# Optimization experiments

Hardware: AMD Instinct MI355X
Metric: run time of the kernel (lower is better)

## Reference

```python
import jax, jax.numpy as jnp
import numpy as np

K = 49        # k_neighbors
EPS = 1e-5    # BatchNorm2d eps


def setup_inputs() -> dict:
    key = jax.random.key(0)
    ks = jax.random.split(key, 2)
    B, C, M, O = 64, 64, 32, 128
    X = jax.random.normal(ks[0], (B, C, M, M), dtype=jnp.float32)
    # conv1x1 weight (kaiming fan_out) flattened to (O, C); bias init 0
    W = jax.random.normal(ks[1], (O, C), dtype=jnp.float32) * (2.0 / O) ** 0.5
    b = jnp.zeros((O,), jnp.float32)
    gamma = jnp.ones((O,), jnp.float32)
    beta = jnp.zeros((O,), jnp.float32)
    run_mean = jnp.zeros((O,), jnp.float32)
    run_var = jnp.ones((O,), jnp.float32)
    return dict(X=X, W=W, b=b, gamma=gamma, beta=beta,
                run_mean=run_mean, run_var=run_var)


def _knn_aggregate(x):
    """x: (N, C) node features -> D^{-1/2} A D^{-1/2} x for the kNN graph."""
    N = x.shape[0]
    sq = jnp.sum(x * x, axis=1)
    d2 = sq[:, None] + sq[None, :] - 2.0 * (x @ x.T)
    dist = jnp.sqrt(jnp.maximum(d2, 0.0))              # torch.cdist (p=2)
    i = jnp.arange(N)
    dist = dist.at[i, i].set(jnp.inf)                  # fill_diagonal_(inf)
    _, knn = jax.lax.top_k(-dist, K)                   # (N, K) nearest indices
    # topk indices are distinct -> every row degree == K, and the column
    # normalizer uses the col node's row degree (also K), so
    # D^{-1/2} A D^{-1/2} x == mean of gathered neighbors.
    nb = x[knn]                                        # (N, K, C) gather
    return nb.sum(axis=1) / K


def reference(X, W, b, gamma, beta, run_mean, run_var):
    B, C, M, _ = X.shape
    N = M * M
    x = X.reshape(B, C, N).transpose(0, 2, 1)          # (B, N, C) nodes
    Z = jax.vmap(_knn_aggregate)(x)                    # (B, N, C) sparse GCN agg
    # 1x1 conv over the (M, M) grid == per-node linear map
    Fg = jnp.einsum('oc,bnc->bon', W, Z) + b[None, :, None]   # (B, O, N)
    Fg = jax.nn.relu(Fg)
    # BatchNorm2d with running stats (eval mode); Dropout2d is identity in eval
    inv = jax.lax.rsqrt(run_var + EPS)
    Fg = gamma[None, :, None] * (Fg - run_mean[None, :, None]) * inv[None, :, None] + beta[None, :, None]
    return Fg.mean(axis=2)                             # AdaptiveAvgPool2d(1) -> (B, O)
```

## Files before the change

kernel.cpp:

```cpp
#include <hip/hip_runtime.h>
#include <stdint.h>

#define BATCH 64
#define CDIM  64
#define NPTS  1024
#define ODIM  128
#define KNN   49
#define KNNP  52
#define BNEPS 1e-5f

typedef __attribute__((ext_vector_type(8))) short bf16x8;
typedef __attribute__((ext_vector_type(4))) float f32x4;

#define O_XF   0
#define SZ_XF  (BATCH*64*2*64*8*4)
#define O_SQ   (O_XF + SZ_XF)
#define SZ_SQ  (BATCH*NPTS*4)
#define O_KNN  (O_SQ + SZ_SQ)
#define SZ_KNN (BATCH*NPTS*KNNP*4)
#define O_Z    (O_KNN + SZ_KNN)
#define SZ_Z   (BATCH*NPTS*CDIM*4)
#define WS_NEED ((size_t)(O_Z + SZ_Z))

__global__ void gcn_init(const float* __restrict__ gamma, const float* __restrict__ beta,
                         const float* __restrict__ rmean, const float* __restrict__ rvar,
                         float* __restrict__ out) {
    int i = blockIdx.x * 256 + threadIdx.x;
    if (i < BATCH * ODIM) {
        int o = i & (ODIM - 1);
        out[i] = beta[o] - gamma[o] * rmean[o] * rsqrtf(rvar[o] + BNEPS);
    }
}

__global__ __launch_bounds__(256) void k0_split(const float* __restrict__ X,
                                                uint32_t* __restrict__ XF,
                                                float* __restrict__ sq) {
    const int b    = blockIdx.x >> 4;
    const int t16  = (blockIdx.x & 15) * 4 + (threadIdx.x >> 6);
    const int lane = threadIdx.x & 63;
    const int n    = t16 * 16 + (lane & 15);
    const int cg   = lane >> 4;
    const float* Xb = X + (size_t)b * CDIM * NPTS;
    float s = 0.f;
    for (int ks = 0; ks < 2; ks++) {
        uint32_t hi[4], lo[4];
#pragma unroll
        for (int dj = 0; dj < 4; dj++) {
            uint32_t hw[2], lw[2];
#pragma unroll
            for (int e = 0; e < 2; e++) {
                int c = ks * 32 + cg * 8 + dj * 2 + e;
                float x = Xb[(size_t)c * NPTS + n];
                s += x * x;
                uint32_t u  = __float_as_uint(x);
                uint32_t hr = (u + 0x7FFFu + ((u >> 16) & 1u)) >> 16;
                float    hf = __uint_as_float(hr << 16);
                uint32_t ul = __float_as_uint(x - hf);
                uint32_t lr = (ul + 0x7FFFu + ((ul >> 16) & 1u)) >> 16;
                hw[e] = hr; lw[e] = lr;
            }
            hi[dj] = hw[0] | (hw[1] << 16);
            lo[dj] = lw[0] | (lw[1] << 16);
        }
        size_t entry = ((size_t)(b * 64 + t16) * 2 + ks) * 64 + lane;
        uint32_t* p = XF + entry * 8;
        *(uint4*)p       = make_uint4(hi[0], hi[1], hi[2], hi[3]);
        *(uint4*)(p + 4) = make_uint4(lo[0], lo[1], lo[2], lo[3]);
    }
    s += __shfl_xor(s, 16, 64);
    s += __shfl_xor(s, 32, 64);
    if (lane < 16) sq[b * NPTS + n] = s;
}

__global__ __launch_bounds__(256, 4) void k1_gram_select(const uint32_t* __restrict__ XF,
                                                         const float* __restrict__ sq,
                                                         int* __restrict__ knn) {
    __shared__ uint32_t s_pk[8 * 1024];
    const int b    = blockIdx.x >> 6;
    const int rt   = blockIdx.x & 63;
    const int wave = threadIdx.x >> 6, lane = threadIdx.x & 63;
    const int q = lane >> 4, l15 = lane & 15;

    bf16x8 ahi[2], alo[2];
#pragma unroll
    for (int ks = 0; ks < 2; ks++) {
        const uint32_t* p = XF + (((size_t)(b * 64 + rt) * 2 + ks) * 64 + lane) * 8;
        ahi[ks] = *(const bf16x8*)p;
        alo[ks] = *(const bf16x8*)(p + 4);
    }
    const float* sqb = sq + b * NPTS;
    const int swq = (q & 1) << 4;

#pragma unroll
    for (int tt = 0; tt < 16; tt++) {
        const int t16 = wave * 16 + tt;
        f32x4 acc = {0.f, 0.f, 0.f, 0.f};
#pragma unroll
        for (int ks = 0; ks < 2; ks++) {
            const uint32_t* p = XF + (((size_t)(b * 64 + t16) * 2 + ks) * 64 + lane) * 8;
            bf16x8 bhi = *(const bf16x8*)p;
            bf16x8 blo = *(const bf16x8*)(p + 4);
            acc = __builtin_amdgcn_mfma_f32_16x16x32_bf16(ahi[ks], bhi, acc, 0, 0, 0);
            acc = __builtin_amdgcn_mfma_f32_16x16x32_bf16(alo[ks], bhi, acc, 0, 0, 0);
            acc = __builtin_amdgcn_mfma_f32_16x16x32_bf16(ahi[ks], blo, acc, 0, 0, 0);
        }
        const int col  = t16 * 16 + l15;
        const float sqv = sqb[col];
        float d[4];
#pragma unroll
        for (int i = 0; i < 4; i++)
            d[i] = fmaf(-2.f, acc[i], sqv);
        if (t16 == rt) {
#pragma unroll
            for (int i = 0; i < 4; i++)
                if (l15 == q * 4 + i) d[i] = __uint_as_float(0x7F800000u);
        }
        uint32_t key[4];
#pragma unroll
        for (int i = 0; i < 4; i++) {
            uint32_t u = __float_as_uint(d[i]);
            key[i] = u ^ (uint32_t)(((int)u >> 31) | 0x80000000);
        }
        uint32_t pk01 = __builtin_amdgcn_perm(key[1], key[0], 0x07060302);
        uint32_t pk23 = __builtin_amdgcn_perm(key[3], key[2], 0x07060302);
        s_pk[(2 * q) * 1024 + (col ^ swq)]     = pk01;
        s_pk[(2 * q + 1) * 1024 + (col ^ swq)] = pk23;
    }
    __syncthreads();

    uint32_t k[4][16];
    {
        const int swr = (wave & 1) << 4;
#pragma unroll
        for (int tt = 0; tt < 16; tt++) {
            uint32_t a  = s_pk[(2 * wave) * 1024 + ((tt * 64 + lane) ^ swr)];
            uint32_t bb = s_pk[(2 * wave + 1) * 1024 + ((tt * 64 + lane) ^ swr)];
            k[0][tt] = a & 0xFFFFu;  k[1][tt] = a >> 16;
            k[2][tt] = bb & 0xFFFFu; k[3][tt] = bb >> 16;
        }
    }

    uint32_t lo[4], hi[4];
    {
        uint32_t lmin[4];
#pragma unroll
        for (int r = 0; r < 4; r++) {
            uint32_t m = k[r][0];
#pragma unroll
            for (int tt = 1; tt < 16; tt++) m = k[r][tt] < m ? k[r][tt] : m;
            lmin[r] = m;
        }
#pragma unroll
        for (int r = 0; r < 4; r++) { lo[r] = lmin[r]; hi[r] = lmin[r]; }
#pragma unroll
        for (int off = 1; off < 64; off <<= 1) {
#pragma unroll
            for (int r = 0; r < 4; r++) {
                uint32_t a = (uint32_t)__shfl_xor((int)lo[r], off, 64);
                uint32_t m = (uint32_t)__shfl_xor((int)hi[r], off, 64);
                lo[r] = a < lo[r] ? a : lo[r];
                hi[r] = m > hi[r] ? m : hi[r];
            }
        }
    }

    for (int it = 0; it < 16; it++) {
        bool act0 = lo[0] < hi[0], act1 = lo[1] < hi[1];
        bool act2 = lo[2] < hi[2], act3 = lo[3] < hi[3];
        if (!act0 && !act1 && !act2 && !act3) break;
        uint32_t mid[4];
        int cnt[4] = {0, 0, 0, 0};
#pragma unroll
        for (int r = 0; r < 4; r++) mid[r] = (lo[r] + hi[r]) >> 1;
#pragma unroll
        for (int tt = 0; tt < 16; tt++) {
            cnt[0] += __popcll(__ballot(k[0][tt] <= mid[0]));
            cnt[1] += __popcll(__ballot(k[1][tt] <= mid[1]));
            cnt[2] += __popcll(__ballot(k[2][tt] <= mid[2]));
            cnt[3] += __popcll(__ballot(k[3][tt] <= mid[3]));
        }
#pragma unroll
        for (int r = 0; r < 4; r++)
            if (lo[r] < hi[r]) {
                if (cnt[r] >= KNN) hi[r] = mid[r]; else lo[r] = mid[r] + 1;
            }
    }

#pragma unroll
    for (int r = 0; r < 4; r++) {
        const uint32_t vstar = lo[r];
        int loc_lt = 0, loc_eq = 0;
#pragma unroll
        for (int tt = 0; tt < 16; tt++) {
            loc_lt += (k[r][tt] < vstar);
            loc_eq += (k[r][tt] == vstar);
        }
        uint32_t v = (uint32_t)loc_lt | ((uint32_t)loc_eq << 16);
#pragma unroll
        for (int off = 1; off < 64; off <<= 1) {
            uint32_t u = (uint32_t)__shfl_up((int)v, off, 64);
            if (lane >= off) v += u;
        }
        uint32_t tot = (uint32_t)__shfl((int)v, 63, 64);
        const int total_lt = (int)(tot & 0xFFFFu);
        int p_lt = (int)(v & 0xFFFFu) - loc_lt;
        int p_eq = total_lt + ((int)(v >> 16) - loc_eq);
        int* kout = knn + ((size_t)b * NPTS + rt * 16 + 4 * wave + r) * KNNP;
#pragma unroll
        for (int tt = 0; tt < 16; tt++) {
            bool islt = k[r][tt] < vstar;
            bool iseq = k[r][tt] == vstar;
            int pos = islt ? p_lt : p_eq;
            bool wv = islt || (iseq && p_eq < KNN);
            if (wv) kout[pos] = tt * 64 + lane;
            p_lt += islt; p_eq += iseq;
        }
    }
}

__global__ __launch_bounds__(512) void k2a_aggregate(const float* __restrict__ X,
                                                     const int* __restrict__ knn,
                                                     float* __restrict__ z) {
    __shared__ float XT[16 * 1024];
    const int b = blockIdx.x >> 2, cg = blockIdx.x & 3;
    const int t = threadIdx.x;
    const float* Xb = X + ((size_t)b * CDIM + cg * 16) * NPTS;
#pragma unroll
    for (int nn = 0; nn < 2; nn++) {
        int n = nn * 512 + t;
#pragma unroll
        for (int g = 0; g < 4; g++) {
            float4 v;
            v.x = Xb[(size_t)(4 * g + 0) * NPTS + n];
            v.y = Xb[(size_t)(4 * g + 1) * NPTS + n];
            v.z = Xb[(size_t)(4 * g + 2) * NPTS + n];
            v.w = Xb[(size_t)(4 * g + 3) * NPTS + n];
            int qp = g ^ ((n >> 1) & 3);
            *(float4*)&XT[n * 16 + qp * 4] = v;
        }
    }
    __syncthreads();
    const int wave = t >> 6, lane = t & 63;
    const int r2 = lane >> 4, kb = (lane >> 2) & 3, g = lane & 3;
    for (int rr = 0; rr < 32; rr++) {
        const int row = wave * 128 + rr * 4 + r2;
        const int* kr = knn + ((size_t)b * NPTS + row) * KNNP;
        float4 s = {0.f, 0.f, 0.f, 0.f};
#pragma unroll
        for (int cs = 0; cs < 3; cs++) {
            int4 j4 = *(const int4*)&kr[(kb + 4 * cs) * 4];
            int js[4] = {j4.x, j4.y, j4.z, j4.w};
#pragma unroll
            for (int e = 0; e < 4; e++) {
                int j = js[e];
                float4 v = *(const float4*)&XT[j * 16 + ((g ^ ((j >> 1) & 3)) << 2)];
                s.x += v.x; s.y += v.y; s.z += v.z; s.w += v.w;
            }
        }
        if (kb == 0) {
            int j = kr[48];
            float4 v = *(const float4*)&XT[j * 16 + ((g ^ ((j >> 1) & 3)) << 2)];
            s.x += v.x; s.y += v.y; s.z += v.z; s.w += v.w;
        }
#pragma unroll
        for (int off = 4; off <= 8; off <<= 1) {
            s.x += __shfl_xor(s.x, off, 64);
            s.y += __shfl_xor(s.y, off, 64);
            s.z += __shfl_xor(s.z, off, 64);
            s.w += __shfl_xor(s.w, off, 64);
        }
        if (kb == 0)
            *(float4*)&z[((size_t)b * NPTS + row) * CDIM + cg * 16 + g * 4] = s;
    }
}

__global__ __launch_bounds__(256) void k2b_gemm(const float* __restrict__ z,
                                                const float* __restrict__ W,
                                                const float* __restrict__ bias,
                                                const float* __restrict__ gamma,
                                                const float* __restrict__ rvar,
                                                float* __restrict__ out) {
    __shared__ __align__(16) float s_zz[128 * 64];
    __shared__ float s_red[2][256];
    const int b = blockIdx.x >> 3, nq = blockIdx.x & 7;
    const int t = threadIdx.x;
    const float* zb = z + ((size_t)b * NPTS + nq * 128) * CDIM;
#pragma unroll
    for (int qq = 0; qq < 8; qq++) {
        int e = qq * 256 + t;
        *(float4*)&s_zz[e * 4] = *(const float4*)&zb[e * 4];
    }
    __syncthreads();
    const int o2 = t & 63, h = t >> 6;
    float4 w0[16], w1[16];
#pragma unroll
    for (int c4 = 0; c4 < 16; c4++) {
        w0[c4] = *(const float4*)&W[(size_t)o2 * CDIM + c4 * 4];
        w1[c4] = *(const float4*)&W[(size_t)(o2 + 64) * CDIM + c4 * 4];
    }
    const float b0 = bias[o2], b1 = bias[o2 + 64];
    float r0 = 0.f, r1 = 0.f;
    for (int r = 0; r < 32; r++) {
        const float* zr = &s_zz[(h * 32 + r) * 64];
        float a0 = 0.f, a1 = 0.f;
#pragma unroll
        for (int c4 = 0; c4 < 16; c4++) {
            float4 zv = *(const float4*)&zr[c4 * 4];
            a0 += w0[c4].x * zv.x + w0[c4].y * zv.y + w0[c4].z * zv.z + w0[c4].w * zv.w;
            a1 += w1[c4].x * zv.x + w1[c4].y * zv.y + w1[c4].z * zv.z + w1[c4].w * zv.w;
        }
        r0 += fmaxf(a0 * (1.f / KNN) + b0, 0.f);
        r1 += fmaxf(a1 * (1.f / KNN) + b1, 0.f);
    }
    s_red[0][t] = r0; s_red[1][t] = r1;
    __syncthreads();
    if (t < 128) {
        const int oo = t & 63, which = t >> 6;
        const int o = which * 64 + oo;
        float sum = s_red[which][oo] + s_red[which][64 + oo] +
                    s_red[which][128 + oo] + s_red[which][192 + oo];
        float scale = gamma[o] * rsqrtf(rvar[o] + BNEPS) * (1.f / NPTS);
        atomicAdd(&out[b * ODIM + o], sum * scale);
    }
}

#define RTILE 8
#define APAD  1028
#define WPAD  132
#define POOLF (64 * WPAD)

__global__ __launch_bounds__(256) void gcn_main(
    const float* __restrict__ X, const float* __restrict__ W,
    const float* __restrict__ bias, const float* __restrict__ gamma,
    const float* __restrict__ rvar, float* __restrict__ out)
{
    __shared__ __align__(16) float s_pool[POOLF];
    __shared__ __align__(16) float s_fstage[4][APAD];
    __shared__ int   s_knn[RTILE][KNN];
    __shared__ float s_z[RTILE][CDIM];

    const int t = threadIdx.x;
    const int b = blockIdx.x >> 7;
    const int rtile = blockIdx.x & 127;
    const int r0 = rtile * RTILE;
    const float* Xb = X + (size_t)b * CDIM * NPTS;

    float acc[RTILE][4];
    float sqv[4];
#pragma unroll
    for (int r = 0; r < RTILE; r++)
#pragma unroll
        for (int u = 0; u < 4; u++) acc[r][u] = 0.f;
#pragma unroll
    for (int u = 0; u < 4; u++) sqv[u] = 0.f;

    for (int ch = 0; ch < 16; ch++) {
        const int c0 = ch * 4;
#pragma unroll
        for (int cc = 0; cc < 4; cc++) {
            float4 v = *(const float4*)(Xb + (size_t)(c0 + cc) * NPTS + 4 * t);
            *(float4*)&s_fstage[cc][4 * t] = v;
        }
        __syncthreads();
#pragma unroll
        for (int cc = 0; cc < 4; cc++) {
            float4 bv4 = *(const float4*)&s_fstage[cc][4 * t];
            float bv[4] = {bv4.x, bv4.y, bv4.z, bv4.w};
#pragma unroll
            for (int u = 0; u < 4; u++) sqv[u] += bv[u] * bv[u];
            const float* arow = Xb + (size_t)(c0 + cc) * NPTS + r0;
            float4 a0 = *(const float4*)(arow);
            float4 a1 = *(const float4*)(arow + 4);
            float av[8] = {a0.x, a0.y, a0.z, a0.w, a1.x, a1.y, a1.z, a1.w};
#pragma unroll
            for (int r = 0; r < RTILE; r++)
#pragma unroll
                for (int u = 0; u < 4; u++) acc[r][u] += av[r] * bv[u];
        }
        __syncthreads();
    }

    float* s_dist = s_pool;
#pragma unroll
    for (int r = 0; r < RTILE; r++) {
        const int rG = r0 + r;
        float d[4];
#pragma unroll
        for (int u = 0; u < 4; u++) {
            float dd = sqv[u] - 2.f * acc[r][u];
            d[u] = (4 * t + u == rG) ? __uint_as_float(0x7F800000u) : dd;
        }
        *(float4*)&s_dist[r * NPTS + 4 * t] = make_float4(d[0], d[1], d[2], d[3]);
    }
    __syncthreads();

    const int wave = t >> 6, lane = t & 63;
    const unsigned long long ltmask = (1ull << lane) - 1ull;
    for (int rr = 0; rr < 2; rr++) {
        const int row = wave * 2 + rr;
        unsigned key[16];
#pragma unroll
        for (int tt = 0; tt < 16; tt++) {
            unsigned u = __float_as_uint(s_dist[row * NPTS + tt * 64 + lane]);
            key[tt] = (u & 0x80000000u) ? ~u : (u | 0x80000000u);
        }
        unsigned lo = 0u, hi = 0xFFFFFFFFu;
        while (lo < hi) {
            unsigned mid = lo + ((hi - lo) >> 1);
            int cnt = 0;
#pragma unroll
            for (int tt = 0; tt < 16; tt++)
                cnt += __popcll(__ballot(key[tt] <= mid));
            if (cnt >= KNN) hi = mid; else lo = mid + 1;
        }
        const unsigned v49 = lo;
        int cntless = 0;
#pragma unroll
        for (int tt = 0; tt < 16; tt++)
            cntless += __popcll(__ballot(key[tt] < v49));
        const int need = KNN - cntless;
        int base = 0, eqtaken = 0;
#pragma unroll
        for (int tt = 0; tt < 16; tt++) {
            bool islt = key[tt] < v49;
            bool iseq = key[tt] == v49;
            unsigned long long meq = __ballot(iseq);
            int eqrank = eqtaken + __popcll(meq & ltmask);
            bool sel = islt || (iseq && (eqrank < need));
            unsigned long long msel = __ballot(sel);
            if (sel) {
                int pos = base + __popcll(msel & ltmask);
                s_knn[row][pos] = tt * 64 + lane;
            }
            base    += __popcll(msel);
            eqtaken += __popcll(meq);
        }
    }
    __syncthreads();

    float* astage = s_pool;
    float* s_redf = (float*)s_fstage;
    const int ar = t >> 5, acc8 = (t & 31) >> 2, ks = t & 3;
    for (int c0 = 0; c0 < CDIM; c0 += 8) {
#pragma unroll
        for (int qq = 0; qq < 8; qq++) {
            int if4 = qq * 256 + t;
            int cc = if4 >> 8, j4 = if4 & 255;
            float4 v = *(const float4*)(Xb + (size_t)(c0 + cc) * NPTS + 4 * j4);
            *(float4*)&astage[cc * APAD + 4 * j4] = v;
        }
        __syncthreads();
        float partial = 0.f;
        for (int k = ks; k < KNN; k += 4)
            partial += astage[acc8 * APAD + s_knn[ar][k]];
        s_redf[t] = partial;
        __syncthreads();
        if (t < 64) {
            int r = t >> 3, cc = t & 7;
            int bi = r * 32 + cc * 4;
            s_z[r][c0 + cc] = s_redf[bi] + s_redf[bi + 1] + s_redf[bi + 2] + s_redf[bi + 3];
        }
        __syncthreads();
    }

    float* wt = s_pool;
#pragma unroll 4
    for (int qq = 0; qq < 32; qq++) {
        int e = qq * 256 + t;
        int o = e >> 6, c = e & 63;
        wt[c * WPAD + o] = W[e];
    }
    __syncthreads();
    const int o = t & 127, rg = t >> 7;
    float facc[4] = {0.f, 0.f, 0.f, 0.f};
    for (int c = 0; c < CDIM; c += 4) {
        float w0 = wt[(c + 0) * WPAD + o], w1 = wt[(c + 1) * WPAD + o];
        float w2 = wt[(c + 2) * WPAD + o], w3 = wt[(c + 3) * WPAD + o];
#pragma unroll
        for (int qq = 0; qq < 4; qq++) {
            float4 zv = *(const float4*)&s_z[rg * 4 + qq][c];
            facc[qq] += w0 * zv.x + w1 * zv.y + w2 * zv.z + w3 * zv.w;
        }
    }
    const float bo = bias[o];
    float rsum = 0.f;
#pragma unroll
    for (int qq = 0; qq < 4; qq++) {
        float f = facc[qq] * (1.f / KNN) + bo;
        rsum += fmaxf(f, 0.f);
    }
    s_redf[t] = rsum;
    __syncthreads();
    if (t < 128) {
        float scale = gamma[t] * rsqrtf(rvar[t] + BNEPS) * (1.f / NPTS);
        atomicAdd(&out[b * ODIM + t], (s_redf[t] + s_redf[t + 128]) * scale);
    }
}

extern "C" void kernel_launch(void* const* d_in, const int* in_sizes, int n_in,
                              void* d_out, int out_size, void* d_ws, size_t ws_size,
                              hipStream_t stream) {
    const float* X     = (const float*)d_in[0];
    const float* W     = (const float*)d_in[1];
    const float* bias  = (const float*)d_in[2];
    const float* gamma = (const float*)d_in[3];
    const float* beta  = (const float*)d_in[4];
    const float* rmean = (const float*)d_in[5];
    const float* rvar  = (const float*)d_in[6];
    float* out = (float*)d_out;

    gcn_init<<<(BATCH * ODIM + 255) / 256, 256, 0, stream>>>(gamma, beta, rmean, rvar, out);
    if (ws_size >= WS_NEED) {
        uint8_t* ws = (uint8_t*)d_ws;
        uint32_t* XF  = (uint32_t*)(ws + O_XF);
        float*    sqw = (float*)(ws + O_SQ);
        int*      knn = (int*)(ws + O_KNN);
        float*    zw  = (float*)(ws + O_Z);
        k0_split<<<BATCH * 16, 256, 0, stream>>>(X, XF, sqw);
        k1_gram_select<<<BATCH * 64, 256, 0, stream>>>(XF, sqw, knn);
        k2a_aggregate<<<BATCH * 4, 512, 0, stream>>>(X, knn, zw);
        k2b_gemm<<<BATCH * 8, 256, 0, stream>>>(zw, W, bias, gamma, rvar, out);
    } else {
        gcn_main<<<BATCH * (NPTS / RTILE), 256, 0, stream>>>(X, W, bias, gamma, rvar, out);
    }
}
```

Measured before the change: 285.7 us.

## Fuse aggregate+GEMM, merge init into split, widen gram-select blocks with ballot-based emit

Folds the output-initialisation kernel into k0_split and fuses the neighbour aggregation with the 1x1-conv GEMM, so the Z intermediate no longer round-trips through global memory. k1_gram_select now handles two 16-row tiles per 512-thread block, which reuses the loaded B fragments across both tiles. Its index emission changes from a shuffle prefix scan to ballot/mbcnt positions, staged in LDS and written out with coalesced int4 stores. The trade-off is that the fused kernel reloads X once per 8-channel slice and does more serial work per block.

```diff
diff --git a/kernel.cpp b/kernel.cpp
--- a/kernel.cpp
+++ b/kernel.cpp
@@ -12,15 +12,18 @@
 typedef __attribute__((ext_vector_type(8))) short bf16x8;
 typedef __attribute__((ext_vector_type(4))) float f32x4;
 
+__device__ __forceinline__ int mbcnt64(unsigned long long m) {
+    return __builtin_amdgcn_mbcnt_hi((uint32_t)(m >> 32),
+           __builtin_amdgcn_mbcnt_lo((uint32_t)m, 0));
+}
+
 #define O_XF   0
 #define SZ_XF  (BATCH*64*2*64*8*4)
 #define O_SQ   (O_XF + SZ_XF)
 #define SZ_SQ  (BATCH*NPTS*4)
 #define O_KNN  (O_SQ + SZ_SQ)
 #define SZ_KNN (BATCH*NPTS*KNNP*4)
-#define O_Z    (O_KNN + SZ_KNN)
-#define SZ_Z   (BATCH*NPTS*CDIM*4)
-#define WS_NEED ((size_t)(O_Z + SZ_Z))
+#define WS_NEED ((size_t)(O_KNN + SZ_KNN))
 
 __global__ void gcn_init(const float* __restrict__ gamma, const float* __restrict__ beta,
                          const float* __restrict__ rmean, const float* __restrict__ rvar,
@@ -34,7 +37,17 @@
 
 __global__ __launch_bounds__(256) void k0_split(const float* __restrict__ X,
                                                 uint32_t* __restrict__ XF,
-                                                float* __restrict__ sq) {
+                                                float* __restrict__ sq,
+                                                const float* __restrict__ gamma,
+                                                const float* __restrict__ beta,
+                                                const float* __restrict__ rmean,
+                                                const float* __restrict__ rvar,
+                                                float* __restrict__ out) {
+    if (blockIdx.x < 32) {
+        int i = blockIdx.x * 256 + threadIdx.x;
+        int o = i & (ODIM - 1);
+        out[i] = beta[o] - gamma[o] * rmean[o] * rsqrtf(rvar[o] + BNEPS);
+    }
     const int b    = blockIdx.x >> 4;
     const int t16  = (blockIdx.x & 15) * 4 + (threadIdx.x >> 6);
     const int lane = threadIdx.x & 63;
@@ -72,86 +85,92 @@
     if (lane < 16) sq[b * NPTS + n] = s;
 }
 
-__global__ __launch_bounds__(256, 4) void k1_gram_select(const uint32_t* __restrict__ XF,
-                                                         const float* __restrict__ sq,
-                                                         int* __restrict__ knn) {
-    __shared__ uint32_t s_pk[8 * 1024];
-    const int b    = blockIdx.x >> 6;
-    const int rt   = blockIdx.x & 63;
+__global__ __launch_bounds__(512) void k1_gram_select(const uint32_t* __restrict__ XF,
+                                                      const float* __restrict__ sq,
+                                                      int* __restrict__ knn) {
+    __shared__ uint32_t s_pk[16 * 1024];
+    const int b    = blockIdx.x >> 5;
+    const int rt   = blockIdx.x & 31;
     const int wave = threadIdx.x >> 6, lane = threadIdx.x & 63;
     const int q = lane >> 4, l15 = lane & 15;
 
-    bf16x8 ahi[2], alo[2];
-#pragma unroll
-    for (int ks = 0; ks < 2; ks++) {
-        const uint32_t* p = XF + (((size_t)(b * 64 + rt) * 2 + ks) * 64 + lane) * 8;
-        ahi[ks] = *(const bf16x8*)p;
-        alo[ks] = *(const bf16x8*)(p + 4);
-    }
+    bf16x8 ahi[2][2], alo[2][2];
+#pragma unroll
+    for (int s = 0; s < 2; s++)
+#pragma unroll
+        for (int ks = 0; ks < 2; ks++) {
+            const uint32_t* p = XF + (size_t)((b * 64 + rt * 2 + s) * 2 + ks) * 512 + lane * 8;
+            ahi[s][ks] = *(const bf16x8*)p;
+            alo[s][ks] = *(const bf16x8*)(p + 4);
+        }
     const float* sqb = sq + b * NPTS;
-    const int swq = (q & 1) << 4;
-
-#pragma unroll
-    for (int tt = 0; tt < 16; tt++) {
-        const int t16 = wave * 16 + tt;
-        f32x4 acc = {0.f, 0.f, 0.f, 0.f};
-#pragma unroll
-        for (int ks = 0; ks < 2; ks++) {
-            const uint32_t* p = XF + (((size_t)(b * 64 + t16) * 2 + ks) * 64 + lane) * 8;
-            bf16x8 bhi = *(const bf16x8*)p;
-            bf16x8 blo = *(const bf16x8*)(p + 4);
-            acc = __builtin_amdgcn_mfma_f32_16x16x32_bf16(ahi[ks], bhi, acc, 0, 0, 0);
-            acc = __builtin_amdgcn_mfma_f32_16x16x32_bf16(alo[ks], bhi, acc, 0, 0, 0);
-            acc = __builtin_amdgcn_mfma_f32_16x16x32_bf16(ahi[ks], blo, acc, 0, 0, 0);
-        }
+
+#pragma unroll
+    for (int tt = 0; tt < 8; tt++) {
+        const int t16 = wave * 8 + tt;
+        const uint32_t* pB = XF + (size_t)((b * 64 + t16) * 2) * 512 + lane * 8;
+        bf16x8 bhi0 = *(const bf16x8*)pB;
+        bf16x8 blo0 = *(const bf16x8*)(pB + 4);
+        bf16x8 bhi1 = *(const bf16x8*)(pB + 512);
+        bf16x8 blo1 = *(const bf16x8*)(pB + 516);
         const int col  = t16 * 16 + l15;
         const float sqv = sqb[col];
-        float d[4];
-#pragma unroll
-        for (int i = 0; i < 4; i++)
-            d[i] = fmaf(-2.f, acc[i], sqv);
-        if (t16 == rt) {
+#pragma unroll
+        for (int s = 0; s < 2; s++) {
+            f32x4 acc = {0.f, 0.f, 0.f, 0.f};
+            acc = __builtin_amdgcn_mfma_f32_16x16x32_bf16(ahi[s][0], bhi0, acc, 0, 0, 0);
+            acc = __builtin_amdgcn_mfma_f32_16x16x32_bf16(alo[s][0], bhi0, acc, 0, 0, 0);
+            acc = __builtin_amdgcn_mfma_f32_16x16x32_bf16(ahi[s][0], blo0, acc, 0, 0, 0);
+            acc = __builtin_amdgcn_mfma_f32_16x16x32_bf16(ahi[s][1], bhi1, acc, 0, 0, 0);
+            acc = __builtin_amdgcn_mfma_f32_16x16x32_bf16(alo[s][1], bhi1, acc, 0, 0, 0);
+            acc = __builtin_amdgcn_mfma_f32_16x16x32_bf16(ahi[s][1], blo1, acc, 0, 0, 0);
+            float d[4];
 #pragma unroll
             for (int i = 0; i < 4; i++)
-                if (l15 == q * 4 + i) d[i] = __uint_as_float(0x7F800000u);
-        }
-        uint32_t key[4];
-#pragma unroll
-        for (int i = 0; i < 4; i++) {
-            uint32_t u = __float_as_uint(d[i]);
-            key[i] = u ^ (uint32_t)(((int)u >> 31) | 0x80000000);
-        }
-        uint32_t pk01 = __builtin_amdgcn_perm(key[1], key[0], 0x07060302);
-        uint32_t pk23 = __builtin_amdgcn_perm(key[3], key[2], 0x07060302);
-        s_pk[(2 * q) * 1024 + (col ^ swq)]     = pk01;
-        s_pk[(2 * q + 1) * 1024 + (col ^ swq)] = pk23;
+                d[i] = fmaf(-2.f, acc[i], sqv);
+            if (t16 == rt * 2 + s) {
+#pragma unroll
+                for (int i = 0; i < 4; i++)
+                    if (l15 == q * 4 + i) d[i] = __uint_as_float(0x7F800000u);
+            }
+            uint32_t key[4];
+#pragma unroll
+            for (int i = 0; i < 4; i++) {
+                uint32_t u = __float_as_uint(d[i]);
+                key[i] = ((int)u < 0) ? ~u : (u | 0x80000000u);
+            }
+            uint32_t pk01 = __builtin_amdgcn_perm(key[1], key[0], 0x07060302);
+            uint32_t pk23 = __builtin_amdgcn_perm(key[3], key[2], 0x07060302);
+            const int p0 = s * 8 + 2 * q, p1 = p0 + 1;
+            s_pk[p0 * 1024 + (col ^ ((p0 & 3) << 3))] = pk01;
+            s_pk[p1 * 1024 + (col ^ ((p1 & 3) << 3))] = pk23;
+        }
     }
     __syncthreads();
 
     uint32_t k[4][16];
     {
-        const int swr = (wave & 1) << 4;
+        const int p0 = 2 * wave, p1 = 2 * wave + 1;
+        const int sw0 = (p0 & 3) << 3, sw1 = (p1 & 3) << 3;
 #pragma unroll
         for (int tt = 0; tt < 16; tt++) {
-            uint32_t a  = s_pk[(2 * wave) * 1024 + ((tt * 64 + lane) ^ swr)];
-            uint32_t bb = s_pk[(2 * wave + 1) * 1024 + ((tt * 64 + lane) ^ swr)];
+            uint32_t a  = s_pk[p0 * 1024 + ((tt * 64 + lane) ^ sw0)];
+            uint32_t bb = s_pk[p1 * 1024 + ((tt * 64 + lane) ^ sw1)];
             k[0][tt] = a & 0xFFFFu;  k[1][tt] = a >> 16;
             k[2][tt] = bb & 0xFFFFu; k[3][tt] = bb >> 16;
         }
     }
+    __syncthreads();
 
     uint32_t lo[4], hi[4];
     {
-        uint32_t lmin[4];
 #pragma unroll
         for (int r = 0; r < 4; r++) {
             uint32_t m = k[r][0];
 #pragma unroll
             for (int tt = 1; tt < 16; tt++) m = k[r][tt] < m ? k[r][tt] : m;
-            lmin[r] = m;
-        }
-#pragma unroll
-        for (int r = 0; r < 4; r++) { lo[r] = lmin[r]; hi[r] = lmin[r]; }
+            lo[r] = m; hi[r] = m;
+        }
 #pragma unroll
         for (int off = 1; off < 64; off <<= 1) {
 #pragma unroll
@@ -165,9 +184,9 @@
     }
 
     for (int it = 0; it < 16; it++) {
-        bool act0 = lo[0] < hi[0], act1 = lo[1] < hi[1];
-        bool act2 = lo[2] < hi[2], act3 = lo[3] < hi[3];
-        if (!act0 && !act1 && !act2 && !act3) break;
+        bool a0 = lo[0] < hi[0], a1 = lo[1] < hi[1];
+        bool a2 = lo[2] < hi[2], a3 = lo[3] < hi[3];
+        if (!a0 && !a1 && !a2 && !a3) break;
         uint32_t mid[4];
         int cnt[4] = {0, 0, 0, 0};
 #pragma unroll
@@ -186,141 +205,127 @@
             }
     }
 
+    int* eknn = (int*)s_pk;
 #pragma unroll
     for (int r = 0; r < 4; r++) {
+        const int lrow = 4 * wave + r;
         const uint32_t vstar = lo[r];
-        int loc_lt = 0, loc_eq = 0;
-#pragma unroll
-        for (int tt = 0; tt < 16; tt++) {
-            loc_lt += (k[r][tt] < vstar);
-            loc_eq += (k[r][tt] == vstar);
-        }
-        uint32_t v = (uint32_t)loc_lt | ((uint32_t)loc_eq << 16);
-#pragma unroll
-        for (int off = 1; off < 64; off <<= 1) {
-            uint32_t u = (uint32_t)__shfl_up((int)v, off, 64);
-            if (lane >= off) v += u;
-        }
-        uint32_t tot = (uint32_t)__shfl((int)v, 63, 64);
-        const int total_lt = (int)(tot & 0xFFFFu);
-        int p_lt = (int)(v & 0xFFFFu) - loc_lt;
-        int p_eq = total_lt + ((int)(v >> 16) - loc_eq);
-        int* kout = knn + ((size_t)b * NPTS + rt * 16 + 4 * wave + r) * KNNP;
+        int total_lt = 0;
+#pragma unroll
+        for (int tt = 0; tt < 16; tt++)
+            total_lt += __popcll(__ballot(k[r][tt] < vstar));
+        int base_lt = 0, base_eq = total_lt;
 #pragma unroll
         for (int tt = 0; tt < 16; tt++) {
             bool islt = k[r][tt] < vstar;
             bool iseq = k[r][tt] == vstar;
-            int pos = islt ? p_lt : p_eq;
-            bool wv = islt || (iseq && p_eq < KNN);
-            if (wv) kout[pos] = tt * 64 + lane;
-            p_lt += islt; p_eq += iseq;
-        }
-    }
-}
-
-__global__ __launch_bounds__(512) void k2a_aggregate(const float* __restrict__ X,
-                                                     const int* __restrict__ knn,
-                                                     float* __restrict__ z) {
-    __shared__ float XT[16 * 1024];
-    const int b = blockIdx.x >> 2, cg = blockIdx.x & 3;
-    const int t = threadIdx.x;
-    const float* Xb = X + ((size_t)b * CDIM + cg * 16) * NPTS;
-#pragma unroll
-    for (int nn = 0; nn < 2; nn++) {
-        int n = nn * 512 + t;
-#pragma unroll
-        for (int g = 0; g < 4; g++) {
-            float4 v;
-            v.x = Xb[(size_t)(4 * g + 0) * NPTS + n];
-            v.y = Xb[(size_t)(4 * g + 1) * NPTS + n];
-            v.z = Xb[(size_t)(4 * g + 2) * NPTS + n];
-            v.w = Xb[(size_t)(4 * g + 3) * NPTS + n];
-            int qp = g ^ ((n >> 1) & 3);
-            *(float4*)&XT[n * 16 + qp * 4] = v;
-        }
-    }
-    __syncthreads();
-    const int wave = t >> 6, lane = t & 63;
-    const int r2 = lane >> 4, kb = (lane >> 2) & 3, g = lane & 3;
-    for (int rr = 0; rr < 32; rr++) {
-        const int row = wave * 128 + rr * 4 + r2;
-        const int* kr = knn + ((size_t)b * NPTS + row) * KNNP;
-        float4 s = {0.f, 0.f, 0.f, 0.f};
-#pragma unroll
-        for (int cs = 0; cs < 3; cs++) {
-            int4 j4 = *(const int4*)&kr[(kb + 4 * cs) * 4];
-            int js[4] = {j4.x, j4.y, j4.z, j4.w};
-#pragma unroll
-            for (int e = 0; e < 4; e++) {
-                int j = js[e];
-                float4 v = *(const float4*)&XT[j * 16 + ((g ^ ((j >> 1) & 3)) << 2)];
-                s.x += v.x; s.y += v.y; s.z += v.z; s.w += v.w;
-            }
-        }
-        if (kb == 0) {
-            int j = kr[48];
-            float4 v = *(const float4*)&XT[j * 16 + ((g ^ ((j >> 1) & 3)) << 2)];
-            s.x += v.x; s.y += v.y; s.z += v.z; s.w += v.w;
-        }
-#pragma unroll
-        for (int off = 4; off <= 8; off <<= 1) {
-            s.x += __shfl_xor(s.x, off, 64);
-            s.y += __shfl_xor(s.y, off, 64);
-            s.z += __shfl_xor(s.z, off, 64);
-            s.w += __shfl_xor(s.w, off, 64);
-        }
-        if (kb == 0)
-            *(float4*)&z[((size_t)b * NPTS + row) * CDIM + cg * 16 + g * 4] = s;
-    }
-}
-
-__global__ __launch_bounds__(256) void k2b_gemm(const float* __restrict__ z,
+            unsigned long long mlt = __ballot(islt);
+            unsigned long long meq = __ballot(iseq);
+            if (mlt | meq) {
+                int pos = islt ? (base_lt + mbcnt64(mlt)) : (base_eq + mbcnt64(meq));
+                if (islt || (iseq && pos < KNN)) eknn[lrow * KNNP + pos] = tt * 64 + lane;
+            }
+            base_lt += __popcll(mlt);
+            base_eq += __popcll(meq);
+        }
+    }
+    __syncthreads();
+    {
+        const int t = threadIdx.x;
+        int* kbase = knn + ((size_t)b * NPTS + rt * 32) * KNNP;
+        if (t < 416) *(int4*)&kbase[t * 4] = *(const int4*)&eknn[t * 4];
+    }
+}
+
+__global__ __launch_bounds__(256) void k2_fused(const float* __restrict__ X,
+                                                const int* __restrict__ knn,
                                                 const float* __restrict__ W,
                                                 const float* __restrict__ bias,
                                                 const float* __restrict__ gamma,
                                                 const float* __restrict__ rvar,
                                                 float* __restrict__ out) {
-    __shared__ __align__(16) float s_zz[128 * 64];
-    __shared__ float s_red[2][256];
+    __shared__ __align__(16) float XT8[8 * 1024];
+    __shared__ float s_red[256];
     const int b = blockIdx.x >> 3, nq = blockIdx.x & 7;
     const int t = threadIdx.x;
-    const float* zb = z + ((size_t)b * NPTS + nq * 128) * CDIM;
-#pragma unroll
-    for (int qq = 0; qq < 8; qq++) {
-        int e = qq * 256 + t;
-        *(float4*)&s_zz[e * 4] = *(const float4*)&zb[e * 4];
-    }
-    __syncthreads();
-    const int o2 = t & 63, h = t >> 6;
-    float4 w0[16], w1[16];
-#pragma unroll
-    for (int c4 = 0; c4 < 16; c4++) {
-        w0[c4] = *(const float4*)&W[(size_t)o2 * CDIM + c4 * 4];
-        w1[c4] = *(const float4*)&W[(size_t)(o2 + 64) * CDIM + c4 * 4];
-    }
-    const float b0 = bias[o2], b1 = bias[o2 + 64];
-    float r0 = 0.f, r1 = 0.f;
-    for (int r = 0; r < 32; r++) {
-        const float* zr = &s_zz[(h * 32 + r) * 64];
-        float a0 = 0.f, a1 = 0.f;
+    const int rl = t >> 1, gg = t & 1;
+    const int row = nq * 128 + rl;
+    const int* kr = knn + ((size_t)b * NPTS + row) * KNNP;
+    int4 j[13];
+#pragma unroll
+    for (int c = 0; c < 13; c++) j[c] = *(const int4*)&kr[c * 4];
+
+    float4 zacc[8];
+    for (int cg8 = 0; cg8 < 8; cg8++) {
+        __syncthreads();
+        const float* Xc = X + ((size_t)b * CDIM + cg8 * 8) * NPTS;
+#pragma unroll
+        for (int k4 = 0; k4 < 4; k4++) {
+            int n = k4 * 256 + t;
+#pragma unroll
+            for (int g2 = 0; g2 < 2; g2++) {
+                float4 v;
+                v.x = Xc[(size_t)(g2 * 4 + 0) * NPTS + n];
+                v.y = Xc[(size_t)(g2 * 4 + 1) * NPTS + n];
+                v.z = Xc[(size_t)(g2 * 4 + 2) * NPTS + n];
+                v.w = Xc[(size_t)(g2 * 4 + 3) * NPTS + n];
+                int sl = (g2 ^ (n & 1)) << 2;
+                *(float4*)&XT8[n * 8 + sl] = v;
+            }
+        }
+        __syncthreads();
+        float4 s = {0.f, 0.f, 0.f, 0.f};
+#pragma unroll
+        for (int c = 0; c < 12; c++) {
+            int js[4] = {j[c].x, j[c].y, j[c].z, j[c].w};
+#pragma unroll
+            for (int e = 0; e < 4; e++) {
+                int jj = js[e];
+                float4 v = *(const float4*)&XT8[jj * 8 + ((gg ^ (jj & 1)) << 2)];
+                s.x += v.x; s.y += v.y; s.z += v.z; s.w += v.w;
+            }
+        }
+        {
+            int jj = j[12].x;
+            float4 v = *(const float4*)&XT8[jj * 8 + ((gg ^ (jj & 1)) << 2)];
+            s.x += v.x; s.y += v.y; s.z += v.z; s.w += v.w;
+        }
+        zacc[cg8] = s;
+    }
+    __syncthreads();
+    float* ZT = XT8;
+#pragma unroll
+    for (int cg8 = 0; cg8 < 8; cg8++) {
+        int colr = ((cg8 * 8 + gg * 4) + (rl & 15) * 4) & 63;
+        *(float4*)&ZT[rl * 64 + colr] = zacc[cg8];
+    }
+    __syncthreads();
+
+    const int o = t & 127, h = t >> 7;
+    float4 wv[16];
+#pragma unroll
+    for (int c4 = 0; c4 < 16; c4++)
+        wv[c4] = *(const float4*)&W[(size_t)o * CDIM + c4 * 4];
+    const float bo = bias[o];
+    float rsum = 0.f;
+    for (int r = 0; r < 64; r++) {
+        const int zr = h * 64 + r;
+        const float* zrow = &ZT[zr * 64];
+        const int rot = (zr & 15) * 4;
+        float a = 0.f;
 #pragma unroll
         for (int c4 = 0; c4 < 16; c4++) {
-            float4 zv = *(const float4*)&zr[c4 * 4];
-            a0 += w0[c4].x * zv.x + w0[c4].y * zv.y + w0[c4].z * zv.z + w0[c4].w * zv.w;
-            a1 += w1[c4].x * zv.x + w1[c4].y * zv.y + w1[c4].z * zv.z + w1[c4].w * zv.w;
-        }
-        r0 += fmaxf(a0 * (1.f / KNN) + b0, 0.f);
-        r1 += fmaxf(a1 * (1.f / KNN) + b1, 0.f);
-    }
-    s_red[0][t] = r0; s_red[1][t] = r1;
+            float4 zv = *(const float4*)&zrow[(c4 * 4 + rot) & 63];
+            a += wv[c4].x * zv.x + wv[c4].y * zv.y + wv[c4].z * zv.z + wv[c4].w * zv.w;
+        }
+        rsum += fmaxf(a * (1.f / KNN) + bo, 0.f);
+    }
+    s_red[t] = rsum;
     __syncthreads();
     if (t < 128) {
-        const int oo = t & 63, which = t >> 6;
-        const int o = which * 64 + oo;
-        float sum = s_red[which][oo] + s_red[which][64 + oo] +
-                    s_red[which][128 + oo] + s_red[which][192 + oo];
-        float scale = gamma[o] * rsqrtf(rvar[o] + BNEPS) * (1.f / NPTS);
-        atomicAdd(&out[b * ODIM + o], sum * scale);
+        float sum = s_red[t] + s_red[t + 128];
+        float scale = gamma[t] * rsqrtf(rvar[t] + BNEPS) * (1.f / NPTS);
+        atomicAdd(&out[b * ODIM + t], sum * scale);
     }
 }
 
@@ -509,18 +514,16 @@
     const float* rvar  = (const float*)d_in[6];
     float* out = (float*)d_out;
 
-    gcn_init<<<(BATCH * ODIM + 255) / 256, 256, 0, stream>>>(gamma, beta, rmean, rvar, out);
     if (ws_size >= WS_NEED) {
         uint8_t* ws = (uint8_t*)d_ws;
         uint32_t* XF  = (uint32_t*)(ws + O_XF);
         float*    sqw = (float*)(ws + O_SQ);
         int*      knn = (int*)(ws + O_KNN);
-        float*    zw  = (float*)(ws + O_Z);
-        k0_split<<<BATCH * 16, 256, 0, stream>>>(X, XF, sqw);
-        k1_gram_select<<<BATCH * 64, 256, 0, stream>>>(XF, sqw, knn);
-        k2a_aggregate<<<BATCH * 4, 512, 0, stream>>>(X, knn, zw);
-        k2b_gemm<<<BATCH * 8, 256, 0, stream>>>(zw, W, bias, gamma, rvar, out);
+        k0_split<<<BATCH * 16, 256, 0, stream>>>(X, XF, sqw, gamma, beta, rmean, rvar, out);
+        k1_gram_select<<<BATCH * 32, 512, 0, stream>>>(XF, sqw, knn);
+        k2_fused<<<BATCH * 8, 256, 0, stream>>>(X, knn, W, bias, gamma, rvar, out);
     } else {
+        gcn_init<<<(BATCH * ODIM + 255) / 256, 256, 0, stream>>>(gamma, beta, rmean, rvar, out);
         gcn_main<<<BATCH * (NPTS / RTILE), 256, 0, stream>>>(X, W, bias, gamma, rvar, out);
     }
 }
```

Result: faster. 276.6 us (-3.2%).
